# Performance work log

Measured on AMD Instinct MI355X. Metric: run time of the kernel, lower is better.

Reference implementation:

```python
import jax, jax.numpy as jnp
import numpy as np

C_IN = 5
KERNEL = 4
DEPTH = 4
C = C_IN + 3  # original + time + 2 CNN channels


def conv1d(x, w, b):
    # x: (B, Cin, L), w: (Cout, Cin, K) -> (B, Cout, L-K+1), 'VALID' padding as in signatory.Augment defaults
    y = jax.lax.conv_general_dilated(x, w, (1,), 'VALID',
                                     dimension_numbers=('NCH', 'OIH', 'NCH'))
    return y + b[None, :, None]


def augment(inp, w1, b1, w2, b2, w3, b3):
    # inp: (B, L, C_in). Mirrors signatory.Augment with layer_sizes=(8,8,2), kernel_size=4,
    # include_original=True, include_time=True, activation=relu (between layers, not after last).
    B, L, _ = inp.shape
    trunc = KERNEL - 1
    orig = inp[:, trunc:, :]                                   # (B, L-3, C_in)
    time = jnp.linspace(0.0, 1.0, L, dtype=inp.dtype)[trunc:]  # time over original stream, truncated
    time = jnp.broadcast_to(time[None, :, None], (B, L - trunc, 1))
    h = conv1d(inp.transpose(0, 2, 1), w1, b1)   # (B, 8, L-3)
    h = conv1d(jax.nn.relu(h), w2, b2)           # (B, 8, L-3)
    h = conv1d(jax.nn.relu(h), w3, b3)           # (B, 2, L-3)
    return jnp.concatenate([orig, time, h.transpose(0, 2, 1)], axis=2)  # (B, L-3, C)


def signature(path):
    # Truncated path signature, depth 4, basepoint=True (zero basepoint prepended).
    # Chen's relation: sig <- sig (tensor) exp(dx), maintained as per-level tensors.
    B, S, Cc = path.shape
    base = jnp.zeros((B, 1, Cc), path.dtype)
    inc = jnp.diff(jnp.concatenate([base, path], axis=1), axis=1)  # (B, S, C) increments incl. basepoint
    inc = inc.transpose(1, 0, 2)  # (S, B, C) for scan

    def step(carry, dx):
        s1, s2, s3, s4 = carry
        # exp(dx) levels: dx^(k)/k!
        e1 = dx
        e2 = jnp.einsum('bi,bj->bij', dx, dx) / 2.0
        e3 = jnp.einsum('bij,bk->bijk', e2, dx) / 3.0
        e4 = jnp.einsum('bijk,bl->bijkl', e3, dx) / 4.0
        # Chen: (A (x) B)_k = sum_i A_i (x) B_{k-i}, A_0 = B_0 = 1
        n1 = s1 + e1
        n2 = s2 + e2 + jnp.einsum('bi,bj->bij', s1, e1)
        n3 = (s3 + e3 + jnp.einsum('bi,bjk->bijk', s1, e2)
              + jnp.einsum('bij,bk->bijk', s2, e1))
        n4 = (s4 + e4 + jnp.einsum('bi,bjkl->bijkl', s1, e3)
              + jnp.einsum('bij,bkl->bijkl', s2, e2)
              + jnp.einsum('bijk,bl->bijkl', s3, e1))
        return (n1, n2, n3, n4), None

    init = (jnp.zeros((B, Cc), path.dtype),
            jnp.zeros((B, Cc, Cc), path.dtype),
            jnp.zeros((B, Cc, Cc, Cc), path.dtype),
            jnp.zeros((B, Cc, Cc, Cc, Cc), path.dtype))
    (s1, s2, s3, s4), _ = jax.lax.scan(step, init, inc)
    return jnp.concatenate([s1.reshape(B, -1), s2.reshape(B, -1),
                            s3.reshape(B, -1), s4.reshape(B, -1)], axis=1)  # (B, 4680)


def setup_inputs() -> dict:
    key = jax.random.key(0)
    ks = jax.random.split(key, 4)
    B, L = 64, 256

    def init_conv(k, cout, cin, ksz):
        bound = 1.0 / np.sqrt(cin * ksz)
        kw, kb = jax.random.split(k)
        w = jax.random.uniform(kw, (cout, cin, ksz), jnp.float32, -bound, bound)
        b = jax.random.uniform(kb, (cout,), jnp.float32, -bound, bound)
        return w, b

    w1, b1 = init_conv(ks[1], 8, C_IN, KERNEL)
    w2, b2 = init_conv(ks[2], 8, 8, 1)
    w3, b3 = init_conv(ks[3], 2, 8, 1)
    inp = jax.random.normal(ks[0], (B, L, C_IN), jnp.float32)
    return {"inp": inp, "w1": w1, "b1": b1, "w2": w2, "b2": b2, "w3": w3, "b3": b3}


def reference(inp, w1, b1, w2, b2, w3, b3):
    x = augment(inp, w1, b1, w2, b2, w3, b3)  # (B, L-3, C)
    return signature(x)                       # (B, 4680)
```

## Files before the change

### kernel.cpp

```cpp
#include <hip/hip_runtime.h>

#define L_IN    256
#define S_STEPS 253
#define CIN     5

__global__ __launch_bounds__(256) void fused_sig_kernel(
    const float* __restrict__ inp,
    const float* __restrict__ w1, const float* __restrict__ b1,
    const float* __restrict__ w2, const float* __restrict__ b2,
    const float* __restrict__ w3, const float* __restrict__ b3,
    float* __restrict__ out)
{
    const int blk = blockIdx.x;
    const int b   = blk >> 1;
    const int tid = threadIdx.x;

    __shared__ float path[S_STEPS][8];
    __shared__ __align__(16) float dxs[264][8];

    const int t = tid;
    if (t < S_STEPS) {
        const float* __restrict__ x = inp + b * (L_IN * CIN);
        float h1[8];
        #pragma unroll
        for (int o = 0; o < 8; ++o) h1[o] = b1[o];
        #pragma unroll
        for (int kk = 0; kk < 4; ++kk) {
            #pragma unroll
            for (int ci = 0; ci < CIN; ++ci) {
                float v = x[(t + kk) * CIN + ci];
                #pragma unroll
                for (int o = 0; o < 8; ++o) h1[o] = fmaf(v, w1[o * 20 + ci * 4 + kk], h1[o]);
            }
        }
        float r1[8];
        #pragma unroll
        for (int o = 0; o < 8; ++o) r1[o] = h1[o] > 0.f ? h1[o] : 0.f;
        float h2[8];
        #pragma unroll
        for (int o = 0; o < 8; ++o) h2[o] = b2[o];
        #pragma unroll
        for (int p = 0; p < 8; ++p) {
            #pragma unroll
            for (int o = 0; o < 8; ++o) h2[o] = fmaf(r1[p], w2[o * 8 + p], h2[o]);
        }
        float r2[8];
        #pragma unroll
        for (int o = 0; o < 8; ++o) r2[o] = h2[o] > 0.f ? h2[o] : 0.f;
        float h30 = b3[0], h31 = b3[1];
        #pragma unroll
        for (int p = 0; p < 8; ++p) {
            h30 = fmaf(r2[p], w3[p], h30);
            h31 = fmaf(r2[p], w3[8 + p], h31);
        }
        #pragma unroll
        for (int c = 0; c < 5; ++c) path[t][c] = x[(t + 3) * CIN + c];
        path[t][5] = (float)(t + 3) * (1.0f / 255.0f);
        path[t][6] = h30;
        path[t][7] = h31;
    }
    if (tid < 88) {
        dxs[S_STEPS + (tid >> 3)][tid & 7] = 0.f;
    }
    __syncthreads();
    if (t < S_STEPS) {
        #pragma unroll
        for (int c = 0; c < 8; ++c) {
            float prev = (t > 0) ? path[t - 1][c] : 0.f;
            dxs[t][c] = path[t][c] - prev;
        }
    }
    __syncthreads();

    const int wave = __builtin_amdgcn_readfirstlane(tid >> 6);
    const int i    = ((blk & 1) << 2) | wave;
    const int lane = tid & 63;
    const int j    = lane >> 3;
    const int k    = lane & 7;

    float s1 = 0.f, s2 = 0.f, s3 = 0.f;
    float s4[8];
    #pragma unroll
    for (int l = 0; l < 8; ++l) s4[l] = 0.f;

    const float4* __restrict__ dx4 = reinterpret_cast<const float4*>(&dxs[0][0]);

    float a_p[4], own_p[4], bb_p[4];
    float4 r0_p[4], r1_p[4];
    #pragma unroll
    for (int u = 0; u < 4; ++u) {
        a_p[u]   = dxs[u][i];
        own_p[u] = dxs[u][k];
        bb_p[u]  = dxs[u][j];
        r0_p[u]  = dx4[u * 2];
        r1_p[u]  = dx4[u * 2 + 1];
    }

    for (int tb = 0; tb < 256; tb += 4) {
        #pragma unroll
        for (int u = 0; u < 4; ++u) {
            const int tn = tb + u + 4;
            float  a_n   = dxs[tn][i];
            float  own_n = dxs[tn][k];
            float  bb_n  = dxs[tn][j];
            float4 r0_n  = dx4[tn * 2];
            float4 r1_n  = dx4[tn * 2 + 1];

            const float a   = a_p[u];
            const float own = own_p[u];
            const float bb  = bb_p[u];
            const float4 r0 = r0_p[u];
            const float4 r1 = r1_p[u];

            const float t2    = fmaf(a, 0.5f, s1);
            const float t3    = fmaf(s1, 0.5f, a * (1.0f / 6.0f));
            const float t4    = fmaf(s1, (1.0f / 6.0f), a * (1.0f / 24.0f));
            const float coef3 = fmaf(bb, t3, s2);
            const float uu    = fmaf(bb, t4, 0.5f * s2);
            const float coef4 = fmaf(own, uu, s3);
            s4[0] = fmaf(coef4, r0.x, s4[0]);
            s4[1] = fmaf(coef4, r0.y, s4[1]);
            s4[2] = fmaf(coef4, r0.z, s4[2]);
            s4[3] = fmaf(coef4, r0.w, s4[3]);
            s4[4] = fmaf(coef4, r1.x, s4[4]);
            s4[5] = fmaf(coef4, r1.y, s4[5]);
            s4[6] = fmaf(coef4, r1.z, s4[6]);
            s4[7] = fmaf(coef4, r1.w, s4[7]);
            s3 = fmaf(coef3, own, s3);
            s2 = fmaf(t2, bb, s2);
            s1 += a;

            a_p[u] = a_n; own_p[u] = own_n; bb_p[u] = bb_n;
            r0_p[u] = r0_n; r1_p[u] = r1_n;
        }
    }

    float* __restrict__ ob = out + (size_t)b * 4680;
    if (lane == 0) ob[i] = s1;
    if (k == 0)    ob[8 + i * 8 + j] = s2;
    ob[72 + (i * 8 + j) * 8 + k] = s3;
    float4* o4 = reinterpret_cast<float4*>(ob + 584 + (size_t)((i * 8 + j) * 8 + k) * 8);
    o4[0] = make_float4(s4[0], s4[1], s4[2], s4[3]);
    o4[1] = make_float4(s4[4], s4[5], s4[6], s4[7]);
}

extern "C" void kernel_launch(void* const* d_in, const int* in_sizes, int n_in,
                              void* d_out, int out_size, void* d_ws, size_t ws_size,
                              hipStream_t stream)
{
    const float* inp = (const float*)d_in[0];
    const float* w1  = (const float*)d_in[1];
    const float* b1  = (const float*)d_in[2];
    const float* w2  = (const float*)d_in[3];
    const float* b2  = (const float*)d_in[4];
    const float* w3  = (const float*)d_in[5];
    const float* b3  = (const float*)d_in[6];
    float* out = (float*)d_out;

    fused_sig_kernel<<<128, 256, 0, stream>>>(inp, w1, b1, w2, b2, w3, b3, out);
}
```

Measured before the change: 83.45 us.

## Split work into one-wave blocks per first index, template index to drop a load

The launch changes from 128 blocks of 256 threads to 512 single-wave blocks, each handling one batch and one first tensor index i. Spreading the work over more blocks is meant to use more compute units. Each block now recomputes the conv augmentation and increments for its batch on its own, which is 8x redundant rather than 2x as before. The index i becomes a template parameter, so the per-step a value comes from the already loaded float4 instead of a separate LDS read, saving one LDS load per step.

```diff
diff --git a/kernel.cpp b/kernel.cpp
--- a/kernel.cpp
+++ b/kernel.cpp
@@ -4,80 +4,11 @@
 #define S_STEPS 253
 #define CIN     5
 
-__global__ __launch_bounds__(256) void fused_sig_kernel(
-    const float* __restrict__ inp,
-    const float* __restrict__ w1, const float* __restrict__ b1,
-    const float* __restrict__ w2, const float* __restrict__ b2,
-    const float* __restrict__ w3, const float* __restrict__ b3,
+template<int I>
+__device__ __forceinline__ void scan_and_store(
+    const float (* __restrict__ dxs)[8], int j, int k, int b, int lane,
     float* __restrict__ out)
 {
-    const int blk = blockIdx.x;
-    const int b   = blk >> 1;
-    const int tid = threadIdx.x;
-
-    __shared__ float path[S_STEPS][8];
-    __shared__ __align__(16) float dxs[264][8];
-
-    const int t = tid;
-    if (t < S_STEPS) {
-        const float* __restrict__ x = inp + b * (L_IN * CIN);
-        float h1[8];
-        #pragma unroll
-        for (int o = 0; o < 8; ++o) h1[o] = b1[o];
-        #pragma unroll
-        for (int kk = 0; kk < 4; ++kk) {
-            #pragma unroll
-            for (int ci = 0; ci < CIN; ++ci) {
-                float v = x[(t + kk) * CIN + ci];
-                #pragma unroll
-                for (int o = 0; o < 8; ++o) h1[o] = fmaf(v, w1[o * 20 + ci * 4 + kk], h1[o]);
-            }
-        }
-        float r1[8];
-        #pragma unroll
-        for (int o = 0; o < 8; ++o) r1[o] = h1[o] > 0.f ? h1[o] : 0.f;
-        float h2[8];
-        #pragma unroll
-        for (int o = 0; o < 8; ++o) h2[o] = b2[o];
-        #pragma unroll
-        for (int p = 0; p < 8; ++p) {
-            #pragma unroll
-            for (int o = 0; o < 8; ++o) h2[o] = fmaf(r1[p], w2[o * 8 + p], h2[o]);
-        }
-        float r2[8];
-        #pragma unroll
-        for (int o = 0; o < 8; ++o) r2[o] = h2[o] > 0.f ? h2[o] : 0.f;
-        float h30 = b3[0], h31 = b3[1];
-        #pragma unroll
-        for (int p = 0; p < 8; ++p) {
-            h30 = fmaf(r2[p], w3[p], h30);
-            h31 = fmaf(r2[p], w3[8 + p], h31);
-        }
-        #pragma unroll
-        for (int c = 0; c < 5; ++c) path[t][c] = x[(t + 3) * CIN + c];
-        path[t][5] = (float)(t + 3) * (1.0f / 255.0f);
-        path[t][6] = h30;
-        path[t][7] = h31;
-    }
-    if (tid < 88) {
-        dxs[S_STEPS + (tid >> 3)][tid & 7] = 0.f;
-    }
-    __syncthreads();
-    if (t < S_STEPS) {
-        #pragma unroll
-        for (int c = 0; c < 8; ++c) {
-            float prev = (t > 0) ? path[t - 1][c] : 0.f;
-            dxs[t][c] = path[t][c] - prev;
-        }
-    }
-    __syncthreads();
-
-    const int wave = __builtin_amdgcn_readfirstlane(tid >> 6);
-    const int i    = ((blk & 1) << 2) | wave;
-    const int lane = tid & 63;
-    const int j    = lane >> 3;
-    const int k    = lane & 7;
-
     float s1 = 0.f, s2 = 0.f, s3 = 0.f;
     float s4[8];
     #pragma unroll
@@ -85,32 +16,33 @@
 
     const float4* __restrict__ dx4 = reinterpret_cast<const float4*>(&dxs[0][0]);
 
-    float a_p[4], own_p[4], bb_p[4];
+    float own_p[4], bb_p[4];
     float4 r0_p[4], r1_p[4];
     #pragma unroll
     for (int u = 0; u < 4; ++u) {
-        a_p[u]   = dxs[u][i];
         own_p[u] = dxs[u][k];
         bb_p[u]  = dxs[u][j];
-        r0_p[u]  = dx4[u * 2];
-        r1_p[u]  = dx4[u * 2 + 1];
+        r0_p[u]  = dx4[2 * u];
+        r1_p[u]  = dx4[2 * u + 1];
     }
 
     for (int tb = 0; tb < 256; tb += 4) {
         #pragma unroll
         for (int u = 0; u < 4; ++u) {
             const int tn = tb + u + 4;
-            float  a_n   = dxs[tn][i];
             float  own_n = dxs[tn][k];
             float  bb_n  = dxs[tn][j];
-            float4 r0_n  = dx4[tn * 2];
-            float4 r1_n  = dx4[tn * 2 + 1];
+            float4 r0_n  = dx4[2 * tn];
+            float4 r1_n  = dx4[2 * tn + 1];
 
-            const float a   = a_p[u];
             const float own = own_p[u];
             const float bb  = bb_p[u];
             const float4 r0 = r0_p[u];
             const float4 r1 = r1_p[u];
+            const float a =
+                (I == 0) ? r0.x : (I == 1) ? r0.y : (I == 2) ? r0.z :
+                (I == 3) ? r0.w : (I == 4) ? r1.x : (I == 5) ? r1.y :
+                (I == 6) ? r1.z : r1.w;
 
             const float t2    = fmaf(a, 0.5f, s1);
             const float t3    = fmaf(s1, 0.5f, a * (1.0f / 6.0f));
@@ -130,18 +62,107 @@
             s2 = fmaf(t2, bb, s2);
             s1 += a;
 
-            a_p[u] = a_n; own_p[u] = own_n; bb_p[u] = bb_n;
-            r0_p[u] = r0_n; r1_p[u] = r1_n;
+            own_p[u] = own_n; bb_p[u] = bb_n;
+            r0_p[u] = r0_n;   r1_p[u] = r1_n;
         }
     }
 
     float* __restrict__ ob = out + (size_t)b * 4680;
-    if (lane == 0) ob[i] = s1;
-    if (k == 0)    ob[8 + i * 8 + j] = s2;
-    ob[72 + (i * 8 + j) * 8 + k] = s3;
-    float4* o4 = reinterpret_cast<float4*>(ob + 584 + (size_t)((i * 8 + j) * 8 + k) * 8);
+    if (lane == 0) ob[I] = s1;
+    if (k == 0)    ob[8 + I * 8 + j] = s2;
+    ob[72 + (I * 8 + j) * 8 + k] = s3;
+    float4* o4 = reinterpret_cast<float4*>(ob + 584 + (size_t)((I * 8 + j) * 8 + k) * 8);
     o4[0] = make_float4(s4[0], s4[1], s4[2], s4[3]);
     o4[1] = make_float4(s4[4], s4[5], s4[6], s4[7]);
+}
+
+__global__ __launch_bounds__(64) void fused_sig_kernel(
+    const float* __restrict__ inp,
+    const float* __restrict__ w1, const float* __restrict__ b1,
+    const float* __restrict__ w2, const float* __restrict__ b2,
+    const float* __restrict__ w3, const float* __restrict__ b3,
+    float* __restrict__ out)
+{
+    const int blk = blockIdx.x;
+    const int b   = blk >> 3;
+    const int i   = blk & 7;
+    const int tid = threadIdx.x;
+
+    __shared__ float path[S_STEPS][8];
+    __shared__ __align__(16) float dxs[264][8];
+
+    const float* __restrict__ x = inp + b * (L_IN * CIN);
+    #pragma unroll
+    for (int p = 0; p < 4; ++p) {
+        const int t = tid + p * 64;
+        if (t < S_STEPS) {
+            float h1[8];
+            #pragma unroll
+            for (int o = 0; o < 8; ++o) h1[o] = b1[o];
+            #pragma unroll
+            for (int kk = 0; kk < 4; ++kk) {
+                #pragma unroll
+                for (int ci = 0; ci < CIN; ++ci) {
+                    float v = x[(t + kk) * CIN + ci];
+                    #pragma unroll
+                    for (int o = 0; o < 8; ++o) h1[o] = fmaf(v, w1[o * 20 + ci * 4 + kk], h1[o]);
+                }
+            }
+            float r1v[8];
+            #pragma unroll
+            for (int o = 0; o < 8; ++o) r1v[o] = h1[o] > 0.f ? h1[o] : 0.f;
+            float h2[8];
+            #pragma unroll
+            for (int o = 0; o < 8; ++o) h2[o] = b2[o];
+            #pragma unroll
+            for (int q = 0; q < 8; ++q) {
+                #pragma unroll
+                for (int o = 0; o < 8; ++o) h2[o] = fmaf(r1v[q], w2[o * 8 + q], h2[o]);
+            }
+            float r2v[8];
+            #pragma unroll
+            for (int o = 0; o < 8; ++o) r2v[o] = h2[o] > 0.f ? h2[o] : 0.f;
+            float h30 = b3[0], h31 = b3[1];
+            #pragma unroll
+            for (int q = 0; q < 8; ++q) {
+                h30 = fmaf(r2v[q], w3[q], h30);
+                h31 = fmaf(r2v[q], w3[8 + q], h31);
+            }
+            #pragma unroll
+            for (int c = 0; c < 5; ++c) path[t][c] = x[(t + 3) * CIN + c];
+            path[t][5] = (float)(t + 3) * (1.0f / 255.0f);
+            path[t][6] = h30;
+            path[t][7] = h31;
+        }
+    }
+    dxs[253 + (tid >> 3)][tid & 7] = 0.f;
+    __syncthreads();
+    #pragma unroll
+    for (int p = 0; p < 4; ++p) {
+        const int t = tid + p * 64;
+        if (t < S_STEPS) {
+            #pragma unroll
+            for (int c = 0; c < 8; ++c) {
+                float prev = (t > 0) ? path[t - 1][c] : 0.f;
+                dxs[t][c] = path[t][c] - prev;
+            }
+        }
+    }
+    __syncthreads();
+
+    const int lane = tid;
+    const int j    = lane >> 3;
+    const int k    = lane & 7;
+    switch (i) {
+        case 0: scan_and_store<0>(dxs, j, k, b, lane, out); break;
+        case 1: scan_and_store<1>(dxs, j, k, b, lane, out); break;
+        case 2: scan_and_store<2>(dxs, j, k, b, lane, out); break;
+        case 3: scan_and_store<3>(dxs, j, k, b, lane, out); break;
+        case 4: scan_and_store<4>(dxs, j, k, b, lane, out); break;
+        case 5: scan_and_store<5>(dxs, j, k, b, lane, out); break;
+        case 6: scan_and_store<6>(dxs, j, k, b, lane, out); break;
+        default: scan_and_store<7>(dxs, j, k, b, lane, out); break;
+    }
 }
 
 extern "C" void kernel_launch(void* const* d_in, const int* in_sizes, int n_in,
@@ -157,5 +178,5 @@
     const float* b3  = (const float*)d_in[6];
     float* out = (float*)d_out;
 
-    fused_sig_kernel<<<128, 256, 0, stream>>>(inp, w1, b1, w2, b2, w3, b3, out);
+    fused_sig_kernel<<<512, 64, 0, stream>>>(inp, w1, b1, w2, b2, w3, b3, out);
 }
```

Measured after the change: 85.34 us. 2.3% more time.

## Split signature scan into time chunks combined via Chen's identity

Applied to the files above, without the earlier changes.

Instead of one sequential 256-step scan per wave, each wave processes 32-step time chunks and builds per-chunk depth-1..3 signatures in shared memory. It then combines them with Chen's relation to obtain the level-4 contributions. The grid grows from 128 to 256 blocks, with each block covering two i indices of a batch. This shortens the serial dependency chain and raises parallelism, at the cost of extra per-step work for the chunk level-3 tensors, more shared memory, and a serialized shared-memory reduction across waves.

```diff
diff --git a/kernel.cpp b/kernel.cpp
--- a/kernel.cpp
+++ b/kernel.cpp
@@ -1,147 +1,275 @@
 #include <hip/hip_runtime.h>
 
-#define L_IN    256
-#define S_STEPS 253
-#define CIN     5
-
-__global__ __launch_bounds__(256) void fused_sig_kernel(
+#define L_IN  256
+#define CIN   5
+#define SIG_N 4680
+
+__global__ __launch_bounds__(256, 1) void sig_fused_kernel(
     const float* __restrict__ inp,
     const float* __restrict__ w1, const float* __restrict__ b1,
     const float* __restrict__ w2, const float* __restrict__ b2,
     const float* __restrict__ w3, const float* __restrict__ b3,
     float* __restrict__ out)
 {
-    const int blk = blockIdx.x;
-    const int b   = blk >> 1;
-    const int tid = threadIdx.x;
-
-    __shared__ float path[S_STEPS][8];
-    __shared__ __align__(16) float dxs[264][8];
-
-    const int t = tid;
-    if (t < S_STEPS) {
-        const float* __restrict__ x = inp + b * (L_IN * CIN);
-        float h1[8];
-        #pragma unroll
-        for (int o = 0; o < 8; ++o) h1[o] = b1[o];
-        #pragma unroll
-        for (int kk = 0; kk < 4; ++kk) {
-            #pragma unroll
-            for (int ci = 0; ci < CIN; ++ci) {
-                float v = x[(t + kk) * CIN + ci];
-                #pragma unroll
-                for (int o = 0; o < 8; ++o) h1[o] = fmaf(v, w1[o * 20 + ci * 4 + kk], h1[o]);
-            }
-        }
-        float r1[8];
-        #pragma unroll
-        for (int o = 0; o < 8; ++o) r1[o] = h1[o] > 0.f ? h1[o] : 0.f;
-        float h2[8];
-        #pragma unroll
-        for (int o = 0; o < 8; ++o) h2[o] = b2[o];
-        #pragma unroll
-        for (int p = 0; p < 8; ++p) {
-            #pragma unroll
-            for (int o = 0; o < 8; ++o) h2[o] = fmaf(r1[p], w2[o * 8 + p], h2[o]);
-        }
-        float r2[8];
-        #pragma unroll
-        for (int o = 0; o < 8; ++o) r2[o] = h2[o] > 0.f ? h2[o] : 0.f;
-        float h30 = b3[0], h31 = b3[1];
-        #pragma unroll
-        for (int p = 0; p < 8; ++p) {
-            h30 = fmaf(r2[p], w3[p], h30);
-            h31 = fmaf(r2[p], w3[8 + p], h31);
-        }
-        #pragma unroll
-        for (int c = 0; c < 5; ++c) path[t][c] = x[(t + 3) * CIN + c];
-        path[t][5] = (float)(t + 3) * (1.0f / 255.0f);
-        path[t][6] = h30;
-        path[t][7] = h31;
-    }
-    if (tid < 88) {
-        dxs[S_STEPS + (tid >> 3)][tid & 7] = 0.f;
-    }
-    __syncthreads();
-    if (t < S_STEPS) {
-        #pragma unroll
-        for (int c = 0; c < 8; ++c) {
-            float prev = (t > 0) ? path[t - 1][c] : 0.f;
-            dxs[t][c] = path[t][c] - prev;
-        }
-    }
-    __syncthreads();
-
-    const int wave = __builtin_amdgcn_readfirstlane(tid >> 6);
-    const int i    = ((blk & 1) << 2) | wave;
+    const int blk  = blockIdx.x;
+    const int b    = blk >> 2;
+    const int iq   = blk & 3;
+    const int tid  = threadIdx.x;
+    const int w    = tid >> 6;
     const int lane = tid & 63;
     const int j    = lane >> 3;
     const int k    = lane & 7;
 
-    float s1 = 0.f, s2 = 0.f, s3 = 0.f;
-    float s4[8];
-    #pragma unroll
-    for (int l = 0; l < 8; ++l) s4[l] = 0.f;
+    __shared__ __align__(16) float dxs[264][8];
+    __shared__ __align__(16) float sig3[8][600];
+    __shared__ float acc[1024];
+
+    const float* __restrict__ x = inp + b * (L_IN * CIN);
+    float o[8];
+    if (tid < 253) {
+        float h1[8];
+        #pragma unroll
+        for (int q = 0; q < 8; ++q) h1[q] = b1[q];
+        #pragma unroll
+        for (int kk = 0; kk < 4; ++kk) {
+            #pragma unroll
+            for (int ci = 0; ci < CIN; ++ci) {
+                float v = x[(tid + kk) * CIN + ci];
+                #pragma unroll
+                for (int q = 0; q < 8; ++q) h1[q] = fmaf(v, w1[q * 20 + ci * 4 + kk], h1[q]);
+            }
+        }
+        float r1v[8];
+        #pragma unroll
+        for (int q = 0; q < 8; ++q) r1v[q] = h1[q] > 0.f ? h1[q] : 0.f;
+        float h2[8];
+        #pragma unroll
+        for (int q = 0; q < 8; ++q) h2[q] = b2[q];
+        #pragma unroll
+        for (int p = 0; p < 8; ++p) {
+            #pragma unroll
+            for (int q = 0; q < 8; ++q) h2[q] = fmaf(r1v[p], w2[q * 8 + p], h2[q]);
+        }
+        float r2v[8];
+        #pragma unroll
+        for (int q = 0; q < 8; ++q) r2v[q] = h2[q] > 0.f ? h2[q] : 0.f;
+        float h30 = b3[0], h31 = b3[1];
+        #pragma unroll
+        for (int p = 0; p < 8; ++p) {
+            h30 = fmaf(r2v[p], w3[p], h30);
+            h31 = fmaf(r2v[p], w3[8 + p], h31);
+        }
+        #pragma unroll
+        for (int cc = 0; cc < 5; ++cc) o[cc] = x[(tid + 3) * CIN + cc];
+        o[5] = (float)(tid + 3) * (1.0f / 255.0f);
+        o[6] = h30;
+        o[7] = h31;
+    }
+    if (tid < 88) dxs[253 + (tid >> 3)][tid & 7] = 0.f;
+    #pragma unroll
+    for (int z = 0; z < 4; ++z) acc[tid * 4 + z] = 0.f;
+    if (tid < 253) {
+        #pragma unroll
+        for (int ch = 0; ch < 8; ++ch) dxs[tid][ch] = o[ch];
+    }
+    __syncthreads();
+    float prevr[8];
+    if (tid < 253) {
+        #pragma unroll
+        for (int ch = 0; ch < 8; ++ch) prevr[ch] = (tid > 0) ? dxs[tid - 1][ch] : 0.f;
+    }
+    __syncthreads();
+    if (tid < 253) {
+        #pragma unroll
+        for (int ch = 0; ch < 8; ++ch) dxs[tid][ch] = o[ch] - prevr[ch];
+    }
+    __syncthreads();
 
     const float4* __restrict__ dx4 = reinterpret_cast<const float4*>(&dxs[0][0]);
-
-    float a_p[4], own_p[4], bb_p[4];
-    float4 r0_p[4], r1_p[4];
-    #pragma unroll
-    for (int u = 0; u < 4; ++u) {
-        a_p[u]   = dxs[u][i];
-        own_p[u] = dxs[u][k];
-        bb_p[u]  = dxs[u][j];
-        r0_p[u]  = dx4[u * 2];
-        r1_p[u]  = dx4[u * 2 + 1];
-    }
-
-    for (int tb = 0; tb < 256; tb += 4) {
-        #pragma unroll
-        for (int u = 0; u < 4; ++u) {
-            const int tn = tb + u + 4;
-            float  a_n   = dxs[tn][i];
-            float  own_n = dxs[tn][k];
-            float  bb_n  = dxs[tn][j];
-            float4 r0_n  = dx4[tn * 2];
-            float4 r1_n  = dx4[tn * 2 + 1];
-
-            const float a   = a_p[u];
-            const float own = own_p[u];
-            const float bb  = bb_p[u];
-            const float4 r0 = r0_p[u];
-            const float4 r1 = r1_p[u];
-
-            const float t2    = fmaf(a, 0.5f, s1);
-            const float t3    = fmaf(s1, 0.5f, a * (1.0f / 6.0f));
-            const float t4    = fmaf(s1, (1.0f / 6.0f), a * (1.0f / 24.0f));
-            const float coef3 = fmaf(bb, t3, s2);
-            const float uu    = fmaf(bb, t4, 0.5f * s2);
-            const float coef4 = fmaf(own, uu, s3);
-            s4[0] = fmaf(coef4, r0.x, s4[0]);
-            s4[1] = fmaf(coef4, r0.y, s4[1]);
-            s4[2] = fmaf(coef4, r0.z, s4[2]);
-            s4[3] = fmaf(coef4, r0.w, s4[3]);
-            s4[4] = fmaf(coef4, r1.x, s4[4]);
-            s4[5] = fmaf(coef4, r1.y, s4[5]);
-            s4[6] = fmaf(coef4, r1.z, s4[6]);
-            s4[7] = fmaf(coef4, r1.w, s4[7]);
-            s3 = fmaf(coef3, own, s3);
-            s2 = fmaf(t2, bb, s2);
-            s1 += a;
-
-            a_p[u] = a_n; own_p[u] = own_n; bb_p[u] = bb_n;
-            r0_p[u] = r0_n; r1_p[u] = r1_n;
-        }
-    }
-
-    float* __restrict__ ob = out + (size_t)b * 4680;
-    if (lane == 0) ob[i] = s1;
-    if (k == 0)    ob[8 + i * 8 + j] = s2;
-    ob[72 + (i * 8 + j) * 8 + k] = s3;
-    float4* o4 = reinterpret_cast<float4*>(ob + 584 + (size_t)((i * 8 + j) * 8 + k) * 8);
-    o4[0] = make_float4(s4[0], s4[1], s4[2], s4[3]);
-    o4[1] = make_float4(s4[4], s4[5], s4[6], s4[7]);
+    float s4v[2][2][8];
+    #pragma unroll
+    for (int hh = 0; hh < 2; ++hh)
+        #pragma unroll
+        for (int m = 0; m < 2; ++m)
+            #pragma unroll
+            for (int l = 0; l < 8; ++l) s4v[hh][m][l] = 0.f;
+
+    #pragma unroll
+    for (int half = 0; half < 2; ++half) {
+        const int cc2   = w + 4 * half;
+        const int rbase = cc2 * 32;
+
+        float t1[8], t2s[8], t3s[8];
+        #pragma unroll
+        for (int i = 0; i < 8; ++i) { t1[i] = 0.f; t2s[i] = 0.f; t3s[i] = 0.f; }
+        float u1[2] = {0.f, 0.f}, u2[2] = {0.f, 0.f}, u3[2] = {0.f, 0.f};
+
+        float own_p[2], bb_p[2];
+        float4 r0_p[2], r1_p[2];
+        #pragma unroll
+        for (int u = 0; u < 2; ++u) {
+            own_p[u] = dxs[rbase + u][k];
+            bb_p[u]  = dxs[rbase + u][j];
+            r0_p[u]  = dx4[2 * (rbase + u)];
+            r1_p[u]  = dx4[2 * (rbase + u) + 1];
+        }
+
+        for (int tb = 0; tb < 32; tb += 2) {
+            #pragma unroll
+            for (int u = 0; u < 2; ++u) {
+                const int tn = rbase + tb + u + 2;
+                float  own_n = dxs[tn][k];
+                float  bb_n  = dxs[tn][j];
+                float4 r0_n  = dx4[2 * tn];
+                float4 r1_n  = dx4[2 * tn + 1];
+
+                const float own = own_p[u];
+                const float bb  = bb_p[u];
+                const float4 r0 = r0_p[u];
+                const float4 r1 = r1_p[u];
+                const float rr[8] = { r0.x, r0.y, r0.z, r0.w, r1.x, r1.y, r1.z, r1.w };
+                const float a0 = (iq == 0) ? r0.x : (iq == 1) ? r0.z
+                               : (iq == 2) ? r1.x : r1.z;
+                const float a1 = (iq == 0) ? r0.y : (iq == 1) ? r0.w
+                               : (iq == 2) ? r1.y : r1.w;
+
+                float c4_0, c4_1;
+                {
+                    const float t4 = fmaf(u1[0], (1.0f / 6.0f), a0 * (1.0f / 24.0f));
+                    const float uu = fmaf(bb, t4, 0.5f * u2[0]);
+                    c4_0 = fmaf(own, uu, u3[0]);
+                }
+                {
+                    const float t4 = fmaf(u1[1], (1.0f / 6.0f), a1 * (1.0f / 24.0f));
+                    const float uu = fmaf(bb, t4, 0.5f * u2[1]);
+                    c4_1 = fmaf(own, uu, u3[1]);
+                }
+                #pragma unroll
+                for (int l = 0; l < 8; ++l) {
+                    s4v[half][0][l] = fmaf(c4_0, rr[l], s4v[half][0][l]);
+                    s4v[half][1][l] = fmaf(c4_1, rr[l], s4v[half][1][l]);
+                }
+                {
+                    const float c3 = fmaf(bb, fmaf(u1[0], 0.5f, a0 * (1.0f / 6.0f)), u2[0]);
+                    u3[0] = fmaf(c3, own, u3[0]);
+                    u2[0] = fmaf(fmaf(a0, 0.5f, u1[0]), bb, u2[0]);
+                    u1[0] += a0;
+                }
+                {
+                    const float c3 = fmaf(bb, fmaf(u1[1], 0.5f, a1 * (1.0f / 6.0f)), u2[1]);
+                    u3[1] = fmaf(c3, own, u3[1]);
+                    u2[1] = fmaf(fmaf(a1, 0.5f, u1[1]), bb, u2[1]);
+                    u1[1] += a1;
+                }
+                #pragma unroll
+                for (int i = 0; i < 8; ++i) {
+                    const float a  = rr[i];
+                    const float c3 = fmaf(bb, fmaf(t1[i], 0.5f, a * (1.0f / 6.0f)), t2s[i]);
+                    t3s[i] = fmaf(c3, own, t3s[i]);
+                    t2s[i] = fmaf(fmaf(a, 0.5f, t1[i]), bb, t2s[i]);
+                    t1[i] += a;
+                }
+
+                own_p[u] = own_n; bb_p[u] = bb_n;
+                r0_p[u] = r0_n;   r1_p[u] = r1_n;
+            }
+        }
+
+        if (lane == 0) {
+            #pragma unroll
+            for (int i = 0; i < 8; ++i) sig3[cc2][i] = t1[i];
+        }
+        if (k == 0) {
+            #pragma unroll
+            for (int i = 0; i < 8; ++i) sig3[cc2][8 + i * 8 + j] = t2s[i];
+        }
+        #pragma unroll
+        for (int i = 0; i < 8; ++i) sig3[cc2][72 + (i * 8 + j) * 8 + k] = t3s[i];
+    }
+    __syncthreads();
+
+    const int i0 = 2 * iq;
+    const int i1 = 2 * iq + 1;
+    float p1[2] = {0.f, 0.f}, p2[2] = {0.f, 0.f}, p3[2] = {0.f, 0.f};
+
+    auto combine = [&](int cc) {
+        const float* __restrict__ lp = sig3[cc];
+        const float s1j  = lp[j];
+        const float s1k  = lp[k];
+        const float s2jk = lp[8 + j * 8 + k];
+        #pragma unroll
+        for (int m = 0; m < 2; ++m) {
+            const int i = i0 + m;
+            const float s1i  = lp[i];
+            const float s2ij = lp[8 + i * 8 + j];
+            const float s3i  = lp[72 + (i * 8 + j) * 8 + k];
+            const float np3 = p3[m] + s3i + p1[m] * s2jk + p2[m] * s1k;
+            const float np2 = p2[m] + s2ij + p1[m] * s1j;
+            p3[m] = np3; p2[m] = np2; p1[m] += s1i;
+        }
+    };
+    auto contrib = [&](int cc, int half) {
+        const float* __restrict__ lp = sig3[cc];
+        const float4 s1a = *reinterpret_cast<const float4*>(lp);
+        const float4 s1b = *reinterpret_cast<const float4*>(lp + 4);
+        const float4 s2a = *reinterpret_cast<const float4*>(lp + 8 + k * 8);
+        const float4 s2b = *reinterpret_cast<const float4*>(lp + 8 + k * 8 + 4);
+        const float4 s3a = *reinterpret_cast<const float4*>(lp + 72 + (j * 8 + k) * 8);
+        const float4 s3b = *reinterpret_cast<const float4*>(lp + 72 + (j * 8 + k) * 8 + 4);
+        const float s1r[8] = { s1a.x, s1a.y, s1a.z, s1a.w, s1b.x, s1b.y, s1b.z, s1b.w };
+        const float s2r[8] = { s2a.x, s2a.y, s2a.z, s2a.w, s2b.x, s2b.y, s2b.z, s2b.w };
+        const float s3r[8] = { s3a.x, s3a.y, s3a.z, s3a.w, s3b.x, s3b.y, s3b.z, s3b.w };
+        #pragma unroll
+        for (int m = 0; m < 2; ++m) {
+            #pragma unroll
+            for (int l = 0; l < 8; ++l) {
+                s4v[half][m][l] = fmaf(p1[m], s3r[l],
+                                   fmaf(p2[m], s2r[l],
+                                    fmaf(p3[m], s1r[l], s4v[half][m][l])));
+            }
+        }
+    };
+
+    for (int cc = 0; cc < w; ++cc) combine(cc);
+    contrib(w, 0);
+    for (int cc = w; cc < w + 4; ++cc) combine(cc);
+    contrib(w + 4, 1);
+
+    float* __restrict__ ob = out + (size_t)b * SIG_N;
+    if (w == 3) {
+        combine(7);
+        #pragma unroll
+        for (int m = 0; m < 2; ++m) {
+            const int i = i0 + m;
+            if (lane == 0) ob[i] = p1[m];
+            if (k == 0)    ob[8 + i * 8 + j] = p2[m];
+            ob[72 + (i * 8 + j) * 8 + k] = p3[m];
+        }
+    }
+
+    #pragma unroll
+    for (int ph = 0; ph < 4; ++ph) {
+        if (w == ph) {
+            #pragma unroll
+            for (int m = 0; m < 2; ++m)
+                #pragma unroll
+                for (int l = 0; l < 8; ++l)
+                    acc[l * 128 + m * 64 + lane] += s4v[0][m][l] + s4v[1][m][l];
+        }
+        __syncthreads();
+    }
+
+    {
+        const int m2 = tid >> 7;
+        const int jk = (tid >> 1) & 63;
+        const int lb = (tid & 1) * 4;
+        float4 v;
+        v.x = acc[(lb + 0) * 128 + m2 * 64 + jk];
+        v.y = acc[(lb + 1) * 128 + m2 * 64 + jk];
+        v.z = acc[(lb + 2) * 128 + m2 * 64 + jk];
+        v.w = acc[(lb + 3) * 128 + m2 * 64 + jk];
+        *reinterpret_cast<float4*>(ob + 584 + iq * 1024 + tid * 4) = v;
+    }
 }
 
 extern "C" void kernel_launch(void* const* d_in, const int* in_sizes, int n_in,
@@ -157,5 +285,5 @@
     const float* b3  = (const float*)d_in[6];
     float* out = (float*)d_out;
 
-    fused_sig_kernel<<<128, 256, 0, stream>>>(inp, w1, b1, w2, b2, w3, b3, out);
+    sig_fused_kernel<<<256, 256, 0, stream>>>(inp, w1, b1, w2, b2, w3, b3, out);
 }
```

Result: no change. 83.87 us (+0.5%).
